# Kernel tuning notes

Measured on AMD Instinct MI355X. Metric: run time of the kernel, lower is better.

Reference implementation:

```python
import jax, jax.numpy as jnp
import numpy as np

K = 64
M = 256
V = 5000

def setup_inputs() -> dict:
    key = jax.random.key(0)
    ks = jax.random.split(key, 8)
    feat_x = jax.random.normal(ks[0], (1, V, M), dtype=jnp.float32)
    feat_y = jax.random.normal(ks[1], (1, V, M), dtype=jnp.float32)
    evals_x = jnp.sort(jax.random.uniform(ks[2], (1, K), dtype=jnp.float32))
    evals_y = jnp.sort(jax.random.uniform(ks[3], (1, K), dtype=jnp.float32))
    evecs_trans_x = jax.random.normal(ks[4], (1, K, V), dtype=jnp.float32) / np.sqrt(V)
    evecs_trans_y = jax.random.normal(ks[5], (1, K, V), dtype=jnp.float32) / np.sqrt(V)
    eye = jnp.eye(K, dtype=jnp.float32)
    sqrtMk_x = (eye + 0.05 * jax.random.normal(ks[6], (K, K), dtype=jnp.float32))[None]
    sqrtMk_y = (eye + 0.05 * jax.random.normal(ks[7], (K, K), dtype=jnp.float32))[None]
    return {"feat_x": feat_x, "feat_y": feat_y, "evals_x": evals_x, "evals_y": evals_y,
            "evecs_trans_x": evecs_trans_x, "evecs_trans_y": evecs_trans_y,
            "sqrtMk_x": sqrtMk_x, "sqrtMk_y": sqrtMk_y}

LMBDA = 0.001

def _fmap(fx, fy, ex, ey, tx, ty, sx, sy):
    # squeeze batch dim of 1 (as in torch .squeeze())
    fx, fy = fx[0], fy[0]            # [V, m]
    ex, ey = ex[0], ey[0]            # [k]
    tx, ty = tx[0], ty[0]            # [k, V]
    sx, sy = sx[0], sy[0]            # [k, k]
    A = tx @ fx                      # [k, m] spectral coeffs of feat_x
    B = sy @ (ty @ fy)               # adapt_feature=True: premultiply by sqrtMk_y
    k, m = A.shape
    vec_B = B.T.reshape(m * k, 1)
    At_Ik = jnp.kron(A.T, sy)        # [m*k, k*k] (adapt_feature -> Ik = sqrtMk_y)
    first = At_Ik.T @ At_Ik          # [k^2, k^2]
    # adapt_mask=True branch
    inv_sx = jnp.linalg.inv(sx)
    lx = jnp.diag(ex)
    ly = jnp.diag(ey)
    lx_Ik = jnp.kron(lx @ inv_sx, sy)
    Ik_ly = jnp.kron(inv_sx, sy @ ly)
    Delta = lx_Ik - Ik_ly
    second = Delta.T @ Delta
    rhs = At_Ik.T @ vec_B
    op = first + LMBDA * second
    C = jnp.linalg.solve(op, rhs)
    return C.reshape(k, k).T[None]   # [1, k, k]

def reference(feat_x, feat_y, evals_x, evals_y, evecs_trans_x, evecs_trans_y, sqrtMk_x, sqrtMk_y):
    # bidirectional=False -> only Cxy (Cyx is None in the torch module)
    return _fmap(feat_x, feat_y, evals_x, evals_y, evecs_trans_x, evecs_trans_y, sqrtMk_x, sqrtMk_y)
```

## Files before the change

kernel.cpp:

```cpp
#include <hip/hip_runtime.h>

#define LMBDA 0.001f
#define NS_SY 4
#define NS_G  5
#define NS_SX 5
#define OUTER 3
#define LDP 68

#define WS_A    0
#define WS_FY   16384
#define WS_G1   32768
#define WS_T1   36864
#define WS_R2   40960
#define WS_R4   45056
#define WS_GINV 49152
#define WS_C    53248
#define WS_FYAT 57344

#define FMA4(ar, xs, b) { ar[0]=fmaf((xs),(b).x,ar[0]); ar[1]=fmaf((xs),(b).y,ar[1]); \
                          ar[2]=fmaf((xs),(b).z,ar[2]); ar[3]=fmaf((xs),(b).w,ar[3]); }

template<int SA, int SB>
__device__ __forceinline__ void mm64(const float* __restrict__ A,
                                     const float* __restrict__ B,
                                     int ti, int tj, float a[4][4]) {
    #pragma unroll 4
    for (int k = 0; k < 64; k += 4) {
        float4 av0 = *(const float4*)&A[(4 * ti + 0) * SA + k];
        float4 av1 = *(const float4*)&A[(4 * ti + 1) * SA + k];
        float4 av2 = *(const float4*)&A[(4 * ti + 2) * SA + k];
        float4 av3 = *(const float4*)&A[(4 * ti + 3) * SA + k];
        float4 b0 = *(const float4*)&B[(k + 0) * SB + 4 * tj];
        float4 b1 = *(const float4*)&B[(k + 1) * SB + 4 * tj];
        float4 b2 = *(const float4*)&B[(k + 2) * SB + 4 * tj];
        float4 b3 = *(const float4*)&B[(k + 3) * SB + 4 * tj];
        FMA4(a[0], av0.x, b0); FMA4(a[0], av0.y, b1); FMA4(a[0], av0.z, b2); FMA4(a[0], av0.w, b3);
        FMA4(a[1], av1.x, b0); FMA4(a[1], av1.y, b1); FMA4(a[1], av1.z, b2); FMA4(a[1], av1.w, b3);
        FMA4(a[2], av2.x, b0); FMA4(a[2], av2.y, b1); FMA4(a[2], av2.z, b2); FMA4(a[2], av2.w, b3);
        FMA4(a[3], av3.x, b0); FMA4(a[3], av3.y, b1); FMA4(a[3], av3.z, b2); FMA4(a[3], av3.w, b3);
    }
}

__global__ __launch_bounds__(256) void k1_gemm(
    const float* __restrict__ tx, const float* __restrict__ fx,
    const float* __restrict__ ty, const float* __restrict__ fy,
    float* __restrict__ wsA, float* __restrict__ wsFy)
{
    __shared__ float sT[64 * LDP];
    __shared__ float sF[64 * LDP];
    const int tid = threadIdx.x;
    const int ti = tid >> 4, tj = tid & 15;
    const int mat = blockIdx.x >> 2;
    const int m0 = (blockIdx.x & 3) << 6;
    const float* __restrict__ T = mat ? ty : tx;
    const float* __restrict__ F = mat ? fy : fx;
    float* __restrict__ Out = mat ? wsFy : wsA;

    float acc[4][4];
    #pragma unroll
    for (int r = 0; r < 4; ++r)
        #pragma unroll
        for (int c = 0; c < 4; ++c) acc[r][c] = 0.f;

    for (int sc = blockIdx.y; sc * 64 < 5000; sc += 27) {
        const int v0 = sc << 6;
        int vlen = 5000 - v0; if (vlen > 64) vlen = 64;
        #pragma unroll
        for (int w = 0; w < 4; ++w) {
            const int fidx = tid + (w << 8);
            const int row = fidx >> 4, q = fidx & 15;
            const int vv = q << 2;
            if (vv < vlen) {
                float4 val = *(const float4*)(T + (size_t)row * 5000 + v0 + vv);
                sT[(vv + 0) * LDP + row] = val.x;
                sT[(vv + 1) * LDP + row] = val.y;
                sT[(vv + 2) * LDP + row] = val.z;
                sT[(vv + 3) * LDP + row] = val.w;
            }
            if (row < vlen) {
                *(float4*)&sF[row * LDP + (q << 2)] =
                    *(const float4*)(F + (size_t)(v0 + row) * 256 + m0 + (q << 2));
            }
        }
        __syncthreads();
        for (int v = 0; v < vlen; ++v) {
            float4 av = *(const float4*)&sT[v * LDP + 4 * ti];
            float4 bv = *(const float4*)&sF[v * LDP + 4 * tj];
            FMA4(acc[0], av.x, bv); FMA4(acc[1], av.y, bv);
            FMA4(acc[2], av.z, bv); FMA4(acc[3], av.w, bv);
        }
        __syncthreads();
    }
    #pragma unroll
    for (int r = 0; r < 4; ++r)
        #pragma unroll
        for (int c = 0; c < 4; ++c)
            atomicAdd(&Out[(4 * ti + r) * 256 + m0 + 4 * tj + c], acc[r][c]);
}

__device__ __forceinline__ void ns_invert(float* sM, float* sX, float* sY,
                                          int iters, int ti, int tj,
                                          int tid, float alpha)
{
    for (int idx = tid; idx < 4096; idx += 256) {
        int i = idx >> 6, j = idx & 63;
        sX[i * LDP + j] = (i == j) ? alpha : 0.f;
    }
    __syncthreads();
    for (int it = 0; it < iters; ++it) {
        float y[4][4];
        #pragma unroll
        for (int r = 0; r < 4; ++r)
            #pragma unroll
            for (int c = 0; c < 4; ++c) y[r][c] = 0.f;
        mm64<LDP, LDP>(sM, sX, ti, tj, y);
        #pragma unroll
        for (int r = 0; r < 4; ++r) {
            float4 v = {y[r][0], y[r][1], y[r][2], y[r][3]};
            *(float4*)&sY[(4 * ti + r) * 64 + 4 * tj] = v;
        }
        __syncthreads();
        float z[4][4];
        #pragma unroll
        for (int r = 0; r < 4; ++r)
            #pragma unroll
            for (int c = 0; c < 4; ++c) z[r][c] = 0.f;
        mm64<LDP, 64>(sX, sY, ti, tj, z);
        __syncthreads();
        #pragma unroll
        for (int r = 0; r < 4; ++r) {
            float4 xv = *(const float4*)&sX[(4 * ti + r) * LDP + 4 * tj];
            xv.x = 2.f * xv.x - z[r][0];
            xv.y = 2.f * xv.y - z[r][1];
            xv.z = 2.f * xv.z - z[r][2];
            xv.w = 2.f * xv.w - z[r][3];
            *(float4*)&sX[(4 * ti + r) * LDP + 4 * tj] = xv;
        }
        __syncthreads();
    }
}

__global__ __launch_bounds__(256, 1) void k2_prep(
    const float* __restrict__ wsA, const float* __restrict__ wsFy,
    const float* __restrict__ sx, const float* __restrict__ sy,
    const float* __restrict__ ex, const float* __restrict__ ey,
    float* __restrict__ ws)
{
    extern __shared__ __align__(16) float lds2[];
    const int tid = threadIdx.x;
    const int ti = tid >> 4, tj = tid & 15;
    const int b = blockIdx.x;

    if (b == 0) {
        float* sSy = lds2;
        float* sXx = lds2 + 4352;
        float* sYy = lds2 + 8704;
        float* sH  = lds2 + 12800;
        float* sV  = lds2 + 16896;
        for (int idx = tid; idx < 1024; idx += 256) {
            int i = idx >> 4, j4 = (idx & 15) << 2;
            *(float4*)&sSy[i * LDP + j4] = *(const float4*)&sy[i * 64 + j4];
        }
        if (tid < 64) sV[tid] = ey[tid];
        __syncthreads();
        {
            float h[4][4];
            #pragma unroll
            for (int r = 0; r < 4; ++r)
                #pragma unroll
                for (int c = 0; c < 4; ++c) h[r][c] = 0.f;
            for (int k = 0; k < 64; ++k) {
                float4 av = *(const float4*)&sSy[k * LDP + 4 * ti];
                float4 bv = *(const float4*)&sSy[k * LDP + 4 * tj];
                FMA4(h[0], av.x, bv); FMA4(h[1], av.y, bv);
                FMA4(h[2], av.z, bv); FMA4(h[3], av.w, bv);
            }
            #pragma unroll
            for (int r = 0; r < 4; ++r) {
                float4 v = {h[r][0], h[r][1], h[r][2], h[r][3]};
                *(float4*)&sH[(4 * ti + r) * 64 + 4 * tj] = v;
            }
        }
        __syncthreads();
        ns_invert(sSy, sXx, sYy, NS_SY, ti, tj, tid, 1.0f);
        {
            float h[4][4];
            #pragma unroll
            for (int r = 0; r < 4; ++r)
                #pragma unroll
                for (int c = 0; c < 4; ++c) h[r][c] = 0.f;
            for (int m = 0; m < 64; m += 4) {
                float4 av[4], bv[4];
                #pragma unroll
                for (int r = 0; r < 4; ++r) av[r] = *(const float4*)&sXx[(4 * ti + r) * LDP + m];
                #pragma unroll
                for (int c = 0; c < 4; ++c) bv[c] = *(const float4*)&sXx[(4 * tj + c) * LDP + m];
                #pragma unroll
                for (int r = 0; r < 4; ++r)
                    #pragma unroll
                    for (int c = 0; c < 4; ++c)
                        h[r][c] += av[r].x * bv[c].x + av[r].y * bv[c].y
                                 + av[r].z * bv[c].z + av[r].w * bv[c].w;
            }
            __syncthreads();
            #pragma unroll
            for (int r = 0; r < 4; ++r) {
                float4 v = {h[r][0], h[r][1], h[r][2], h[r][3]};
                *(float4*)&sSy[(4 * ti + r) * LDP + 4 * tj] = v;
            }
        }
        __syncthreads();
        {
            float a[4][4];
            #pragma unroll
            for (int r = 0; r < 4; ++r)
                #pragma unroll
                for (int c = 0; c < 4; ++c) a[r][c] = 0.f;
            #pragma unroll 4
            for (int k = 0; k < 64; k += 4) {
                float4 av[4];
                #pragma unroll
                for (int r = 0; r < 4; ++r) av[r] = *(const float4*)&sSy[(4 * ti + r) * LDP + k];
                #pragma unroll
                for (int q = 0; q < 4; ++q) {
                    float e = sV[k + q];
                    float4 bv = *(const float4*)&sH[(k + q) * 64 + 4 * tj];
                    bv.x *= e; bv.y *= e; bv.z *= e; bv.w *= e;
                    float xq[4] = {av[0].x, av[1].x, av[2].x, av[3].x};
                    if (q == 1) { xq[0]=av[0].y; xq[1]=av[1].y; xq[2]=av[2].y; xq[3]=av[3].y; }
                    if (q == 2) { xq[0]=av[0].z; xq[1]=av[1].z; xq[2]=av[2].z; xq[3]=av[3].z; }
                    if (q == 3) { xq[0]=av[0].w; xq[1]=av[1].w; xq[2]=av[2].w; xq[3]=av[3].w; }
                    #pragma unroll
                    for (int r = 0; r < 4; ++r) FMA4(a[r], xq[r], bv);
                }
            }
            #pragma unroll
            for (int r = 0; r < 4; ++r) {
                float4 v = {a[r][0], a[r][1], a[r][2], a[r][3]};
                *(float4*)&ws[WS_C + (4 * ti + r) * 64 + 4 * tj] = v;
            }
        }
    } else if (b == 1) {
        float* sA = lds2;
        float* sG = lds2 + 4352;
        float* sX = lds2 + 8704;
        float* sY = lds2 + 13056;
        float* sV = lds2 + 17152;
        float a[4][4];
        #pragma unroll
        for (int r = 0; r < 4; ++r)
            #pragma unroll
            for (int c = 0; c < 4; ++c) a[r][c] = 0.f;
        for (int ch = 0; ch < 4; ++ch) {
            for (int idx = tid; idx < 1024; idx += 256) {
                int i = idx >> 4, m4 = (idx & 15) << 2;
                *(float4*)&sA[i * LDP + m4] =
                    *(const float4*)&wsA[i * 256 + (ch << 6) + m4];
            }
            __syncthreads();
            for (int m = 0; m < 64; m += 4) {
                float4 av[4], bv[4];
                #pragma unroll
                for (int r = 0; r < 4; ++r) av[r] = *(const float4*)&sA[(4 * ti + r) * LDP + m];
                #pragma unroll
                for (int c = 0; c < 4; ++c) bv[c] = *(const float4*)&sA[(4 * tj + c) * LDP + m];
                #pragma unroll
                for (int r = 0; r < 4; ++r)
                    #pragma unroll
                    for (int c = 0; c < 4; ++c)
                        a[r][c] += av[r].x * bv[c].x + av[r].y * bv[c].y
                                 + av[r].z * bv[c].z + av[r].w * bv[c].w;
            }
            __syncthreads();
        }
        #pragma unroll
        for (int r = 0; r < 4; ++r) {
            float4 v = {a[r][0], a[r][1], a[r][2], a[r][3]};
            *(float4*)&sG[(4 * ti + r) * LDP + 4 * tj] = v;
            *(float4*)&ws[WS_G1 + (4 * ti + r) * 64 + 4 * tj] = v;
        }
        __syncthreads();
        if (tid < 64) {
            float s = 0.f;
            for (int j4 = 0; j4 < 64; j4 += 4) {
                float4 v = *(const float4*)&sG[tid * LDP + j4];
                s += v.x * v.x + v.y * v.y + v.z * v.z + v.w * v.w;
            }
            sV[tid] = s;
            sV[64 + tid] = sG[tid * LDP + tid];
        }
        __syncthreads();
        float f2 = 0.f, tr = 0.f;
        for (int i = 0; i < 64; ++i) { f2 += sV[i]; tr += sV[64 + i]; }
        ns_invert(sG, sX, sY, NS_G, ti, tj, tid, tr / f2);
        for (int idx = tid; idx < 1024; idx += 256) {
            int i = idx >> 4, j4 = (idx & 15) << 2;
            *(float4*)&ws[WS_GINV + i * 64 + j4] = *(const float4*)&sX[i * LDP + j4];
        }
    } else if (b == 2) {
        float* sM = lds2;
        float* sX = lds2 + 4352;
        float* sY = lds2 + 8704;
        float* sV = lds2 + 12800;
        for (int idx = tid; idx < 1024; idx += 256) {
            int i = idx >> 4, j4 = (idx & 15) << 2;
            *(float4*)&sM[i * LDP + j4] = *(const float4*)&sx[i * 64 + j4];
        }
        if (tid < 64) sV[tid] = ex[tid];
        __syncthreads();
        ns_invert(sM, sX, sY, NS_SX, ti, tj, tid, 1.0f);
        float aR2[4][4], aR4[4][4], aT1[4][4];
        #pragma unroll
        for (int r = 0; r < 4; ++r)
            #pragma unroll
            for (int c = 0; c < 4; ++c) { aR2[r][c] = 0.f; aR4[r][c] = 0.f; aT1[r][c] = 0.f; }
        for (int k = 0; k < 64; ++k) {
            float e = sV[k], e2 = e * e;
            float4 av = *(const float4*)&sX[k * LDP + 4 * ti];
            float4 bv = *(const float4*)&sX[k * LDP + 4 * tj];
            float avv[4] = {av.x, av.y, av.z, av.w};
            #pragma unroll
            for (int r = 0; r < 4; ++r) {
                FMA4(aR4[r], avv[r], bv);
                float ea = e * avv[r];
                FMA4(aR2[r], ea, bv);
                float e2a = e2 * avv[r];
                FMA4(aT1[r], e2a, bv);
            }
        }
        #pragma unroll
        for (int r = 0; r < 4; ++r) {
            int o = (4 * ti + r) * 64 + 4 * tj;
            float4 v2 = {aR2[r][0], aR2[r][1], aR2[r][2], aR2[r][3]};
            float4 v4 = {aR4[r][0], aR4[r][1], aR4[r][2], aR4[r][3]};
            float4 v1 = {aT1[r][0], aT1[r][1], aT1[r][2], aT1[r][3]};
            *(float4*)&ws[WS_R2 + o] = v2;
            *(float4*)&ws[WS_R4 + o] = v4;
            *(float4*)&ws[WS_T1 + o] = v1;
        }
    } else {
        float* sFy = lds2;
        float* sAx = lds2 + 4352;
        float a[4][4];
        #pragma unroll
        for (int r = 0; r < 4; ++r)
            #pragma unroll
            for (int c = 0; c < 4; ++c) a[r][c] = 0.f;
        for (int ch = 0; ch < 4; ++ch) {
            for (int idx = tid; idx < 1024; idx += 256) {
                int i = idx >> 4, m4 = (idx & 15) << 2;
                *(float4*)&sFy[i * LDP + m4] = *(const float4*)&wsFy[i * 256 + (ch << 6) + m4];
                *(float4*)&sAx[i * LDP + m4] = *(const float4*)&wsA[i * 256 + (ch << 6) + m4];
            }
            __syncthreads();
            for (int m = 0; m < 64; m += 4) {
                float4 av[4], bv[4];
                #pragma unroll
                for (int r = 0; r < 4; ++r) av[r] = *(const float4*)&sFy[(4 * ti + r) * LDP + m];
                #pragma unroll
                for (int c = 0; c < 4; ++c) bv[c] = *(const float4*)&sAx[(4 * tj + c) * LDP + m];
                #pragma unroll
                for (int r = 0; r < 4; ++r)
                    #pragma unroll
                    for (int c = 0; c < 4; ++c)
                        a[r][c] += av[r].x * bv[c].x + av[r].y * bv[c].y
                                 + av[r].z * bv[c].z + av[r].w * bv[c].w;
            }
            __syncthreads();
        }
        #pragma unroll
        for (int r = 0; r < 4; ++r) {
            float4 v = {a[r][0], a[r][1], a[r][2], a[r][3]};
            *(float4*)&ws[WS_FYAT + (4 * ti + r) * 64 + 4 * tj] = v;
        }
    }
}

__global__ __launch_bounds__(256, 1) void k3_solve(
    const float* __restrict__ ws, const float* __restrict__ ey_g,
    float* __restrict__ out)
{
    extern __shared__ __align__(16) float lds3[];
    float* cM1   = lds3;
    float* cR2   = lds3 + 4096;
    float* cR4   = lds3 + 8192;
    float* cGinv = lds3 + 12288;
    float* sE    = lds3 + 16384;
    float* sX    = lds3 + 20480;
    float* cC    = lds3 + 24832;
    float* sW    = lds3 + 29184;
    const int tid = threadIdx.x;
    const int ti = tid >> 4, tj = tid & 15;

    for (int idx = tid; idx < 1024; idx += 256) {
        int i = idx >> 4, j4 = (idx & 15) << 2;
        int o = i * 64 + j4;
        float4 g = *(const float4*)&ws[WS_G1 + o];
        float4 t = *(const float4*)&ws[WS_T1 + o];
        float4 m = {fmaf(LMBDA, t.x, g.x), fmaf(LMBDA, t.y, g.y),
                    fmaf(LMBDA, t.z, g.z), fmaf(LMBDA, t.w, g.w)};
        *(float4*)&cM1[o]   = m;
        *(float4*)&cR2[o]   = *(const float4*)&ws[WS_R2 + o];
        *(float4*)&cR4[o]   = *(const float4*)&ws[WS_R4 + o];
        *(float4*)&cGinv[o] = *(const float4*)&ws[WS_GINV + o];
        *(float4*)&cC[i * LDP + j4] = *(const float4*)&ws[WS_C + o];
    }
    float4 eyv = *(const float4*)&ey_g[4 * ti];
    float eyr[4] = {eyv.x, eyv.y, eyv.z, eyv.w};
    float leyr[4];
    #pragma unroll
    for (int r = 0; r < 4; ++r) leyr[r] = LMBDA * eyr[r];

    float fyr[4][4], xreg[4][4];
    #pragma unroll
    for (int r = 0; r < 4; ++r) {
        float4 v = *(const float4*)&ws[WS_FYAT + (4 * ti + r) * 64 + 4 * tj];
        fyr[r][0] = v.x; fyr[r][1] = v.y; fyr[r][2] = v.z; fyr[r][3] = v.w;
        float4 z = {0.f, 0.f, 0.f, 0.f};
        *(float4*)&sX[(4 * ti + r) * LDP + 4 * tj] = z;
        #pragma unroll
        for (int c = 0; c < 4; ++c) xreg[r][c] = 0.f;
    }
    __syncthreads();

    float E1[4][4];
    for (int it = 0; it < OUTER; ++it) {
        {
            float Sm[4][4], S2[4][4], S4[4][4];
            #pragma unroll
            for (int r = 0; r < 4; ++r)
                #pragma unroll
                for (int c = 0; c < 4; ++c) { Sm[r][c] = 0.f; S2[r][c] = 0.f; S4[r][c] = 0.f; }
            #pragma unroll 2
            for (int k = 0; k < 64; k += 4) {
                float4 av[4];
                #pragma unroll
                for (int r = 0; r < 4; ++r)
                    av[r] = *(const float4*)&sX[(4 * ti + r) * LDP + k];
                #pragma unroll
                for (int q = 0; q < 4; ++q) {
                    float4 mv = *(const float4*)&cM1[(k + q) * 64 + 4 * tj];
                    float4 qv = *(const float4*)&cR2[(k + q) * 64 + 4 * tj];
                    float4 rv = *(const float4*)&cR4[(k + q) * 64 + 4 * tj];
                    float xq[4] = {av[0].x, av[1].x, av[2].x, av[3].x};
                    if (q == 1) { xq[0]=av[0].y; xq[1]=av[1].y; xq[2]=av[2].y; xq[3]=av[3].y; }
                    if (q == 2) { xq[0]=av[0].z; xq[1]=av[1].z; xq[2]=av[2].z; xq[3]=av[3].z; }
                    if (q == 3) { xq[0]=av[0].w; xq[1]=av[1].w; xq[2]=av[2].w; xq[3]=av[3].w; }
                    #pragma unroll
                    for (int r = 0; r < 4; ++r) {
                        FMA4(Sm[r], xq[r], mv);
                        FMA4(S2[r], xq[r], qv);
                        FMA4(S4[r], xq[r], rv);
                    }
                }
            }
            #pragma unroll
            for (int r = 0; r < 4; ++r) {
                float4 e2;
                e2.x = LMBDA * fmaf(eyr[r], S4[r][0], -S2[r][0]);
                e2.y = LMBDA * fmaf(eyr[r], S4[r][1], -S2[r][1]);
                e2.z = LMBDA * fmaf(eyr[r], S4[r][2], -S2[r][2]);
                e2.w = LMBDA * fmaf(eyr[r], S4[r][3], -S2[r][3]);
                *(float4*)&sE[(4 * ti + r) * 64 + 4 * tj] = e2;
                #pragma unroll
                for (int c = 0; c < 4; ++c)
                    E1[r][c] = fmaf(-leyr[r], S2[r][c], Sm[r][c]);
            }
        }
        __syncthreads();
        {
            float Z[4][4];
            #pragma unroll
            for (int r = 0; r < 4; ++r)
                #pragma unroll
                for (int c = 0; c < 4; ++c) Z[r][c] = 0.f;
            mm64<LDP, 64>(cC, sE, ti, tj, Z);
            #pragma unroll
            for (int r = 0; r < 4; ++r) {
                float4 w;
                w.x = fyr[r][0] - E1[r][0] - Z[r][0];
                w.y = fyr[r][1] - E1[r][1] - Z[r][1];
                w.z = fyr[r][2] - E1[r][2] - Z[r][2];
                w.w = fyr[r][3] - E1[r][3] - Z[r][3];
                *(float4*)&sW[(4 * ti + r) * LDP + 4 * tj] = w;
            }
        }
        __syncthreads();
        {
            float dX[4][4];
            #pragma unroll
            for (int r = 0; r < 4; ++r)
                #pragma unroll
                for (int c = 0; c < 4; ++c) dX[r][c] = 0.f;
            mm64<LDP, 64>(sW, cGinv, ti, tj, dX);
            #pragma unroll
            for (int r = 0; r < 4; ++r) {
                float4 v;
                #pragma unroll
                for (int c = 0; c < 4; ++c) xreg[r][c] += dX[r][c];
                v.x = xreg[r][0]; v.y = xreg[r][1]; v.z = xreg[r][2]; v.w = xreg[r][3];
                *(float4*)&sX[(4 * ti + r) * LDP + 4 * tj] = v;
                if (it == OUTER - 1)
                    *(float4*)&out[(4 * ti + r) * 64 + 4 * tj] = v;
            }
        }
        if (it == OUTER - 1) break;
        __syncthreads();
    }
}

extern "C" void kernel_launch(void* const* d_in, const int* in_sizes, int n_in,
                              void* d_out, int out_size, void* d_ws, size_t ws_size,
                              hipStream_t stream) {
    (void)in_sizes; (void)n_in; (void)out_size; (void)ws_size;
    const float* fx = (const float*)d_in[0];
    const float* fy = (const float*)d_in[1];
    const float* ex = (const float*)d_in[2];
    const float* ey = (const float*)d_in[3];
    const float* tx = (const float*)d_in[4];
    const float* ty = (const float*)d_in[5];
    const float* sx = (const float*)d_in[6];
    const float* sy = (const float*)d_in[7];
    float* ws = (float*)d_ws;
    float* out = (float*)d_out;

    (void)hipFuncSetAttribute((const void*)k2_prep,
                              hipFuncAttributeMaxDynamicSharedMemorySize, 69120);
    (void)hipFuncSetAttribute((const void*)k3_solve,
                              hipFuncAttributeMaxDynamicSharedMemorySize, 134144);

    (void)hipMemsetAsync(d_ws, 0, 2 * 64 * 256 * sizeof(float), stream);
    k1_gemm<<<dim3(8, 27), 256, 0, stream>>>(tx, fx, ty, fy, ws + WS_A, ws + WS_FY);
    k2_prep<<<4, 256, 69120, stream>>>(ws + WS_A, ws + WS_FY, sx, sy, ex, ey, ws);
    k3_solve<<<1, 256, 134144, stream>>>(ws, ey, out);
}
```

Before: 181.6 us.

## Fuse three kernels into one persistent kernel with flag-based inter-block dependencies

Merges the GEMM, prep and solve kernels into a single 225-block launch whose blocks play different roles and synchronize through global atomic flags with acquire/release spin-waits. Prep work that does not depend on the GEMM (the sy and sx inversion blocks) can now run concurrently with the large reduction, and the two extra kernel launches go away. The Gram matrix G1 is now split across four blocks, one per channel chunk, that accumulate with atomics, instead of being computed serially in one block. This relies on all 225 blocks being co-resident at one block per CU, and adds spin-wait and atomic overhead.

```diff
diff --git a/kernel.cpp b/kernel.cpp
--- a/kernel.cpp
+++ b/kernel.cpp
@@ -16,6 +16,7 @@
 #define WS_GINV 49152
 #define WS_C    53248
 #define WS_FYAT 57344
+#define WS_FLAGS 61440
 
 #define FMA4(ar, xs, b) { ar[0]=fmaf((xs),(b).x,ar[0]); ar[1]=fmaf((xs),(b).y,ar[1]); \
                           ar[2]=fmaf((xs),(b).z,ar[2]); ar[3]=fmaf((xs),(b).w,ar[3]); }
@@ -41,63 +42,6 @@
     }
 }
 
-__global__ __launch_bounds__(256) void k1_gemm(
-    const float* __restrict__ tx, const float* __restrict__ fx,
-    const float* __restrict__ ty, const float* __restrict__ fy,
-    float* __restrict__ wsA, float* __restrict__ wsFy)
-{
-    __shared__ float sT[64 * LDP];
-    __shared__ float sF[64 * LDP];
-    const int tid = threadIdx.x;
-    const int ti = tid >> 4, tj = tid & 15;
-    const int mat = blockIdx.x >> 2;
-    const int m0 = (blockIdx.x & 3) << 6;
-    const float* __restrict__ T = mat ? ty : tx;
-    const float* __restrict__ F = mat ? fy : fx;
-    float* __restrict__ Out = mat ? wsFy : wsA;
-
-    float acc[4][4];
-    #pragma unroll
-    for (int r = 0; r < 4; ++r)
-        #pragma unroll
-        for (int c = 0; c < 4; ++c) acc[r][c] = 0.f;
-
-    for (int sc = blockIdx.y; sc * 64 < 5000; sc += 27) {
-        const int v0 = sc << 6;
-        int vlen = 5000 - v0; if (vlen > 64) vlen = 64;
-        #pragma unroll
-        for (int w = 0; w < 4; ++w) {
-            const int fidx = tid + (w << 8);
-            const int row = fidx >> 4, q = fidx & 15;
-            const int vv = q << 2;
-            if (vv < vlen) {
-                float4 val = *(const float4*)(T + (size_t)row * 5000 + v0 + vv);
-                sT[(vv + 0) * LDP + row] = val.x;
-                sT[(vv + 1) * LDP + row] = val.y;
-                sT[(vv + 2) * LDP + row] = val.z;
-                sT[(vv + 3) * LDP + row] = val.w;
-            }
-            if (row < vlen) {
-                *(float4*)&sF[row * LDP + (q << 2)] =
-                    *(const float4*)(F + (size_t)(v0 + row) * 256 + m0 + (q << 2));
-            }
-        }
-        __syncthreads();
-        for (int v = 0; v < vlen; ++v) {
-            float4 av = *(const float4*)&sT[v * LDP + 4 * ti];
-            float4 bv = *(const float4*)&sF[v * LDP + 4 * tj];
-            FMA4(acc[0], av.x, bv); FMA4(acc[1], av.y, bv);
-            FMA4(acc[2], av.z, bv); FMA4(acc[3], av.w, bv);
-        }
-        __syncthreads();
-    }
-    #pragma unroll
-    for (int r = 0; r < 4; ++r)
-        #pragma unroll
-        for (int c = 0; c < 4; ++c)
-            atomicAdd(&Out[(4 * ti + r) * 256 + m0 + 4 * tj + c], acc[r][c]);
-}
-
 __device__ __forceinline__ void ns_invert(float* sM, float* sX, float* sY,
                                           int iters, int ti, int tj,
                                           int tid, float alpha)
@@ -140,23 +84,134 @@
     }
 }
 
-__global__ __launch_bounds__(256, 1) void k2_prep(
-    const float* __restrict__ wsA, const float* __restrict__ wsFy,
+__device__ __forceinline__ void wait_ge(int* flag, int target, int tid) {
+    if (tid == 0) {
+        while (__hip_atomic_load(flag, __ATOMIC_ACQUIRE, __HIP_MEMORY_SCOPE_AGENT) < target)
+            __builtin_amdgcn_s_sleep(2);
+    }
+    __syncthreads();
+    __threadfence();
+}
+
+__device__ __forceinline__ void signal_one(int* flag, int tid) {
+    __syncthreads();
+    __threadfence();
+    if (tid == 0)
+        (void)__hip_atomic_fetch_add(flag, 1, __ATOMIC_RELEASE, __HIP_MEMORY_SCOPE_AGENT);
+}
+
+__global__ __launch_bounds__(256, 1) void fused_fmnet(
+    const float* __restrict__ fx, const float* __restrict__ fy,
+    const float* __restrict__ ex, const float* __restrict__ ey,
+    const float* __restrict__ tx, const float* __restrict__ ty,
     const float* __restrict__ sx, const float* __restrict__ sy,
-    const float* __restrict__ ex, const float* __restrict__ ey,
-    float* __restrict__ ws)
+    float* __restrict__ ws, float* __restrict__ out)
 {
-    extern __shared__ __align__(16) float lds2[];
+    extern __shared__ __align__(16) float lds[];
+    int* flags = (int*)(ws + WS_FLAGS);
     const int tid = threadIdx.x;
     const int ti = tid >> 4, tj = tid & 15;
-    const int b = blockIdx.x;
-
-    if (b == 0) {
-        float* sSy = lds2;
-        float* sXx = lds2 + 4352;
-        float* sYy = lds2 + 8704;
-        float* sH  = lds2 + 12800;
-        float* sV  = lds2 + 16896;
+    const int bid = blockIdx.x;
+
+    if (bid < 216) {
+        float* sT = lds;
+        float* sF = lds + 4352;
+        const int gx = bid & 7, gy = bid >> 3;
+        const int mat = gx >> 2;
+        const int m0 = (gx & 3) << 6;
+        const float* __restrict__ T = mat ? ty : tx;
+        const float* __restrict__ F = mat ? fy : fx;
+        float* __restrict__ Out = ws + (mat ? WS_FY : WS_A);
+
+        float acc[4][4];
+        #pragma unroll
+        for (int r = 0; r < 4; ++r)
+            #pragma unroll
+            for (int c = 0; c < 4; ++c) acc[r][c] = 0.f;
+
+        for (int sc = gy; sc * 64 < 5000; sc += 27) {
+            const int v0 = sc << 6;
+            int vlen = 5000 - v0; if (vlen > 64) vlen = 64;
+            #pragma unroll
+            for (int w = 0; w < 4; ++w) {
+                const int fidx = tid + (w << 8);
+                const int row = fidx >> 4, q = fidx & 15;
+                const int vv = q << 2;
+                if (vv < vlen) {
+                    float4 val = *(const float4*)(T + (size_t)row * 5000 + v0 + vv);
+                    sT[(vv + 0) * LDP + row] = val.x;
+                    sT[(vv + 1) * LDP + row] = val.y;
+                    sT[(vv + 2) * LDP + row] = val.z;
+                    sT[(vv + 3) * LDP + row] = val.w;
+                }
+                if (row < vlen) {
+                    *(float4*)&sF[row * LDP + (q << 2)] =
+                        *(const float4*)(F + (size_t)(v0 + row) * 256 + m0 + (q << 2));
+                }
+            }
+            __syncthreads();
+            for (int v = 0; v < vlen; ++v) {
+                float4 av = *(const float4*)&sT[v * LDP + 4 * ti];
+                float4 bv = *(const float4*)&sF[v * LDP + 4 * tj];
+                FMA4(acc[0], av.x, bv); FMA4(acc[1], av.y, bv);
+                FMA4(acc[2], av.z, bv); FMA4(acc[3], av.w, bv);
+            }
+            __syncthreads();
+        }
+        #pragma unroll
+        for (int r = 0; r < 4; ++r)
+            #pragma unroll
+            for (int c = 0; c < 4; ++c)
+                atomicAdd(&Out[(4 * ti + r) * 256 + m0 + 4 * tj + c], acc[r][c]);
+        __syncthreads();
+        __threadfence();
+        if (tid == 0) {
+            (void)__hip_atomic_fetch_add(&flags[gx], 1, __ATOMIC_RELEASE, __HIP_MEMORY_SCOPE_AGENT);
+            (void)__hip_atomic_fetch_add(&flags[10], 1, __ATOMIC_RELEASE, __HIP_MEMORY_SCOPE_AGENT);
+        }
+    } else if (bid < 220) {
+        const int ch = bid - 216;
+        wait_ge(&flags[ch], 27, tid);
+        float* sA = lds;
+        for (int idx = tid; idx < 1024; idx += 256) {
+            int i = idx >> 4, m4 = (idx & 15) << 2;
+            *(float4*)&sA[i * LDP + m4] =
+                *(const float4*)&ws[WS_A + i * 256 + (ch << 6) + m4];
+        }
+        __syncthreads();
+        float a[4][4];
+        #pragma unroll
+        for (int r = 0; r < 4; ++r)
+            #pragma unroll
+            for (int c = 0; c < 4; ++c) a[r][c] = 0.f;
+        for (int m = 0; m < 64; m += 4) {
+            float4 av[4], bv[4];
+            #pragma unroll
+            for (int r = 0; r < 4; ++r) av[r] = *(const float4*)&sA[(4 * ti + r) * LDP + m];
+            #pragma unroll
+            for (int c = 0; c < 4; ++c) bv[c] = *(const float4*)&sA[(4 * tj + c) * LDP + m];
+            #pragma unroll
+            for (int r = 0; r < 4; ++r)
+                #pragma unroll
+                for (int c = 0; c < 4; ++c)
+                    a[r][c] += av[r].x * bv[c].x + av[r].y * bv[c].y
+                             + av[r].z * bv[c].z + av[r].w * bv[c].w;
+        }
+        #pragma unroll
+        for (int r = 0; r < 4; ++r)
+            #pragma unroll
+            for (int c = 0; c < 4; ++c)
+                atomicAdd(&ws[WS_G1 + (4 * ti + r) * 64 + 4 * tj + c], a[r][c]);
+        __syncthreads();
+        __threadfence();
+        if (tid == 0)
+            (void)__hip_atomic_fetch_add(&flags[8], 1, __ATOMIC_RELEASE, __HIP_MEMORY_SCOPE_AGENT);
+    } else if (bid == 220) {
+        float* sSy = lds;
+        float* sXx = lds + 4352;
+        float* sYy = lds + 8704;
+        float* sH  = lds + 12800;
+        float* sV  = lds + 16896;
         for (int idx = tid; idx < 1024; idx += 256) {
             int i = idx >> 4, j4 = (idx & 15) << 2;
             *(float4*)&sSy[i * LDP + j4] = *(const float4*)&sy[i * 64 + j4];
@@ -240,68 +295,12 @@
                 *(float4*)&ws[WS_C + (4 * ti + r) * 64 + 4 * tj] = v;
             }
         }
-    } else if (b == 1) {
-        float* sA = lds2;
-        float* sG = lds2 + 4352;
-        float* sX = lds2 + 8704;
-        float* sY = lds2 + 13056;
-        float* sV = lds2 + 17152;
-        float a[4][4];
-        #pragma unroll
-        for (int r = 0; r < 4; ++r)
-            #pragma unroll
-            for (int c = 0; c < 4; ++c) a[r][c] = 0.f;
-        for (int ch = 0; ch < 4; ++ch) {
-            for (int idx = tid; idx < 1024; idx += 256) {
-                int i = idx >> 4, m4 = (idx & 15) << 2;
-                *(float4*)&sA[i * LDP + m4] =
-                    *(const float4*)&wsA[i * 256 + (ch << 6) + m4];
-            }
-            __syncthreads();
-            for (int m = 0; m < 64; m += 4) {
-                float4 av[4], bv[4];
-                #pragma unroll
-                for (int r = 0; r < 4; ++r) av[r] = *(const float4*)&sA[(4 * ti + r) * LDP + m];
-                #pragma unroll
-                for (int c = 0; c < 4; ++c) bv[c] = *(const float4*)&sA[(4 * tj + c) * LDP + m];
-                #pragma unroll
-                for (int r = 0; r < 4; ++r)
-                    #pragma unroll
-                    for (int c = 0; c < 4; ++c)
-                        a[r][c] += av[r].x * bv[c].x + av[r].y * bv[c].y
-                                 + av[r].z * bv[c].z + av[r].w * bv[c].w;
-            }
-            __syncthreads();
-        }
-        #pragma unroll
-        for (int r = 0; r < 4; ++r) {
-            float4 v = {a[r][0], a[r][1], a[r][2], a[r][3]};
-            *(float4*)&sG[(4 * ti + r) * LDP + 4 * tj] = v;
-            *(float4*)&ws[WS_G1 + (4 * ti + r) * 64 + 4 * tj] = v;
-        }
-        __syncthreads();
-        if (tid < 64) {
-            float s = 0.f;
-            for (int j4 = 0; j4 < 64; j4 += 4) {
-                float4 v = *(const float4*)&sG[tid * LDP + j4];
-                s += v.x * v.x + v.y * v.y + v.z * v.z + v.w * v.w;
-            }
-            sV[tid] = s;
-            sV[64 + tid] = sG[tid * LDP + tid];
-        }
-        __syncthreads();
-        float f2 = 0.f, tr = 0.f;
-        for (int i = 0; i < 64; ++i) { f2 += sV[i]; tr += sV[64 + i]; }
-        ns_invert(sG, sX, sY, NS_G, ti, tj, tid, tr / f2);
-        for (int idx = tid; idx < 1024; idx += 256) {
-            int i = idx >> 4, j4 = (idx & 15) << 2;
-            *(float4*)&ws[WS_GINV + i * 64 + j4] = *(const float4*)&sX[i * LDP + j4];
-        }
-    } else if (b == 2) {
-        float* sM = lds2;
-        float* sX = lds2 + 4352;
-        float* sY = lds2 + 8704;
-        float* sV = lds2 + 12800;
+        signal_one(&flags[9], tid);
+    } else if (bid == 221) {
+        float* sM = lds;
+        float* sX = lds + 4352;
+        float* sY = lds + 8704;
+        float* sV = lds + 12800;
         for (int idx = tid; idx < 1024; idx += 256) {
             int i = idx >> 4, j4 = (idx & 15) << 2;
             *(float4*)&sM[i * LDP + j4] = *(const float4*)&sx[i * 64 + j4];
@@ -338,9 +337,40 @@
             *(float4*)&ws[WS_R4 + o] = v4;
             *(float4*)&ws[WS_T1 + o] = v1;
         }
-    } else {
-        float* sFy = lds2;
-        float* sAx = lds2 + 4352;
+        signal_one(&flags[9], tid);
+    } else if (bid == 222) {
+        wait_ge(&flags[8], 4, tid);
+        float* sG = lds;
+        float* sX = lds + 4352;
+        float* sY = lds + 8704;
+        float* sV = lds + 12800;
+        for (int idx = tid; idx < 1024; idx += 256) {
+            int i = idx >> 4, j4 = (idx & 15) << 2;
+            *(float4*)&sG[i * LDP + j4] = *(const float4*)&ws[WS_G1 + i * 64 + j4];
+        }
+        __syncthreads();
+        if (tid < 64) {
+            float s = 0.f;
+            for (int j4 = 0; j4 < 64; j4 += 4) {
+                float4 v = *(const float4*)&sG[tid * LDP + j4];
+                s += v.x * v.x + v.y * v.y + v.z * v.z + v.w * v.w;
+            }
+            sV[tid] = s;
+            sV[64 + tid] = sG[tid * LDP + tid];
+        }
+        __syncthreads();
+        float f2 = 0.f, tr = 0.f;
+        for (int i = 0; i < 64; ++i) { f2 += sV[i]; tr += sV[64 + i]; }
+        ns_invert(sG, sX, sY, NS_G, ti, tj, tid, tr / f2);
+        for (int idx = tid; idx < 1024; idx += 256) {
+            int i = idx >> 4, j4 = (idx & 15) << 2;
+            *(float4*)&ws[WS_GINV + i * 64 + j4] = *(const float4*)&sX[i * LDP + j4];
+        }
+        signal_one(&flags[9], tid);
+    } else if (bid == 223) {
+        wait_ge(&flags[10], 216, tid);
+        float* sFy = lds;
+        float* sAx = lds + 4352;
         float a[4][4];
         #pragma unroll
         for (int r = 0; r < 4; ++r)
@@ -349,8 +379,8 @@
         for (int ch = 0; ch < 4; ++ch) {
             for (int idx = tid; idx < 1024; idx += 256) {
                 int i = idx >> 4, m4 = (idx & 15) << 2;
-                *(float4*)&sFy[i * LDP + m4] = *(const float4*)&wsFy[i * 256 + (ch << 6) + m4];
-                *(float4*)&sAx[i * LDP + m4] = *(const float4*)&wsA[i * 256 + (ch << 6) + m4];
+                *(float4*)&sFy[i * LDP + m4] = *(const float4*)&ws[WS_FY + i * 256 + (ch << 6) + m4];
+                *(float4*)&sAx[i * LDP + m4] = *(const float4*)&ws[WS_A  + i * 256 + (ch << 6) + m4];
             }
             __syncthreads();
             for (int m = 0; m < 64; m += 4) {
@@ -373,139 +403,133 @@
             float4 v = {a[r][0], a[r][1], a[r][2], a[r][3]};
             *(float4*)&ws[WS_FYAT + (4 * ti + r) * 64 + 4 * tj] = v;
         }
-    }
-}
-
-__global__ __launch_bounds__(256, 1) void k3_solve(
-    const float* __restrict__ ws, const float* __restrict__ ey_g,
-    float* __restrict__ out)
-{
-    extern __shared__ __align__(16) float lds3[];
-    float* cM1   = lds3;
-    float* cR2   = lds3 + 4096;
-    float* cR4   = lds3 + 8192;
-    float* cGinv = lds3 + 12288;
-    float* sE    = lds3 + 16384;
-    float* sX    = lds3 + 20480;
-    float* cC    = lds3 + 24832;
-    float* sW    = lds3 + 29184;
-    const int tid = threadIdx.x;
-    const int ti = tid >> 4, tj = tid & 15;
-
-    for (int idx = tid; idx < 1024; idx += 256) {
-        int i = idx >> 4, j4 = (idx & 15) << 2;
-        int o = i * 64 + j4;
-        float4 g = *(const float4*)&ws[WS_G1 + o];
-        float4 t = *(const float4*)&ws[WS_T1 + o];
-        float4 m = {fmaf(LMBDA, t.x, g.x), fmaf(LMBDA, t.y, g.y),
-                    fmaf(LMBDA, t.z, g.z), fmaf(LMBDA, t.w, g.w)};
-        *(float4*)&cM1[o]   = m;
-        *(float4*)&cR2[o]   = *(const float4*)&ws[WS_R2 + o];
-        *(float4*)&cR4[o]   = *(const float4*)&ws[WS_R4 + o];
-        *(float4*)&cGinv[o] = *(const float4*)&ws[WS_GINV + o];
-        *(float4*)&cC[i * LDP + j4] = *(const float4*)&ws[WS_C + o];
-    }
-    float4 eyv = *(const float4*)&ey_g[4 * ti];
-    float eyr[4] = {eyv.x, eyv.y, eyv.z, eyv.w};
-    float leyr[4];
-    #pragma unroll
-    for (int r = 0; r < 4; ++r) leyr[r] = LMBDA * eyr[r];
-
-    float fyr[4][4], xreg[4][4];
-    #pragma unroll
-    for (int r = 0; r < 4; ++r) {
-        float4 v = *(const float4*)&ws[WS_FYAT + (4 * ti + r) * 64 + 4 * tj];
-        fyr[r][0] = v.x; fyr[r][1] = v.y; fyr[r][2] = v.z; fyr[r][3] = v.w;
-        float4 z = {0.f, 0.f, 0.f, 0.f};
-        *(float4*)&sX[(4 * ti + r) * LDP + 4 * tj] = z;
-        #pragma unroll
-        for (int c = 0; c < 4; ++c) xreg[r][c] = 0.f;
-    }
-    __syncthreads();
-
-    float E1[4][4];
-    for (int it = 0; it < OUTER; ++it) {
-        {
-            float Sm[4][4], S2[4][4], S4[4][4];
-            #pragma unroll
-            for (int r = 0; r < 4; ++r)
-                #pragma unroll
-                for (int c = 0; c < 4; ++c) { Sm[r][c] = 0.f; S2[r][c] = 0.f; S4[r][c] = 0.f; }
-            #pragma unroll 2
-            for (int k = 0; k < 64; k += 4) {
-                float4 av[4];
+        signal_one(&flags[9], tid);
+    } else {
+        wait_ge(&flags[9], 4, tid);
+        float* cM1   = lds;
+        float* cR2   = lds + 4096;
+        float* cR4   = lds + 8192;
+        float* cGinv = lds + 12288;
+        float* sE    = lds + 16384;
+        float* sX    = lds + 20480;
+        float* cC    = lds + 24832;
+        float* sW    = lds + 29184;
+
+        for (int idx = tid; idx < 1024; idx += 256) {
+            int i = idx >> 4, j4 = (idx & 15) << 2;
+            int o = i * 64 + j4;
+            float4 g = *(const float4*)&ws[WS_G1 + o];
+            float4 t = *(const float4*)&ws[WS_T1 + o];
+            float4 m = {fmaf(LMBDA, t.x, g.x), fmaf(LMBDA, t.y, g.y),
+                        fmaf(LMBDA, t.z, g.z), fmaf(LMBDA, t.w, g.w)};
+            *(float4*)&cM1[o]   = m;
+            *(float4*)&cR2[o]   = *(const float4*)&ws[WS_R2 + o];
+            *(float4*)&cR4[o]   = *(const float4*)&ws[WS_R4 + o];
+            *(float4*)&cGinv[o] = *(const float4*)&ws[WS_GINV + o];
+            *(float4*)&cC[i * LDP + j4] = *(const float4*)&ws[WS_C + o];
+        }
+        float4 eyv = *(const float4*)&ey[4 * ti];
+        float eyr[4] = {eyv.x, eyv.y, eyv.z, eyv.w};
+        float leyr[4];
+        #pragma unroll
+        for (int r = 0; r < 4; ++r) leyr[r] = LMBDA * eyr[r];
+
+        float fyr[4][4], xreg[4][4];
+        #pragma unroll
+        for (int r = 0; r < 4; ++r) {
+            float4 v = *(const float4*)&ws[WS_FYAT + (4 * ti + r) * 64 + 4 * tj];
+            fyr[r][0] = v.x; fyr[r][1] = v.y; fyr[r][2] = v.z; fyr[r][3] = v.w;
+            float4 z = {0.f, 0.f, 0.f, 0.f};
+            *(float4*)&sX[(4 * ti + r) * LDP + 4 * tj] = z;
+            #pragma unroll
+            for (int c = 0; c < 4; ++c) xreg[r][c] = 0.f;
+        }
+        __syncthreads();
+
+        float E1[4][4];
+        for (int it = 0; it < OUTER; ++it) {
+            {
+                float Sm[4][4], S2[4][4], S4[4][4];
                 #pragma unroll
                 for (int r = 0; r < 4; ++r)
-                    av[r] = *(const float4*)&sX[(4 * ti + r) * LDP + k];
-                #pragma unroll
-                for (int q = 0; q < 4; ++q) {
-                    float4 mv = *(const float4*)&cM1[(k + q) * 64 + 4 * tj];
-                    float4 qv = *(const float4*)&cR2[(k + q) * 64 + 4 * tj];
-                    float4 rv = *(const float4*)&cR4[(k + q) * 64 + 4 * tj];
-                    float xq[4] = {av[0].x, av[1].x, av[2].x, av[3].x};
-                    if (q == 1) { xq[0]=av[0].y; xq[1]=av[1].y; xq[2]=av[2].y; xq[3]=av[3].y; }
-                    if (q == 2) { xq[0]=av[0].z; xq[1]=av[1].z; xq[2]=av[2].z; xq[3]=av[3].z; }
-                    if (q == 3) { xq[0]=av[0].w; xq[1]=av[1].w; xq[2]=av[2].w; xq[3]=av[3].w; }
-                    #pragma unroll
-                    for (int r = 0; r < 4; ++r) {
-                        FMA4(Sm[r], xq[r], mv);
-                        FMA4(S2[r], xq[r], qv);
-                        FMA4(S4[r], xq[r], rv);
+                    #pragma unroll
+                    for (int c = 0; c < 4; ++c) { Sm[r][c] = 0.f; S2[r][c] = 0.f; S4[r][c] = 0.f; }
+                #pragma unroll 2
+                for (int k = 0; k < 64; k += 4) {
+                    float4 av[4];
+                    #pragma unroll
+                    for (int r = 0; r < 4; ++r)
+                        av[r] = *(const float4*)&sX[(4 * ti + r) * LDP + k];
+                    #pragma unroll
+                    for (int q = 0; q < 4; ++q) {
+                        float4 mv = *(const float4*)&cM1[(k + q) * 64 + 4 * tj];
+                        float4 qv = *(const float4*)&cR2[(k + q) * 64 + 4 * tj];
+                        float4 rv = *(const float4*)&cR4[(k + q) * 64 + 4 * tj];
+                        float xq[4] = {av[0].x, av[1].x, av[2].x, av[3].x};
+                        if (q == 1) { xq[0]=av[0].y; xq[1]=av[1].y; xq[2]=av[2].y; xq[3]=av[3].y; }
+                        if (q == 2) { xq[0]=av[0].z; xq[1]=av[1].z; xq[2]=av[2].z; xq[3]=av[3].z; }
+                        if (q == 3) { xq[0]=av[0].w; xq[1]=av[1].w; xq[2]=av[2].w; xq[3]=av[3].w; }
+                        #pragma unroll
+                        for (int r = 0; r < 4; ++r) {
+                            FMA4(Sm[r], xq[r], mv);
+                            FMA4(S2[r], xq[r], qv);
+                            FMA4(S4[r], xq[r], rv);
+                        }
                     }
                 }
-            }
-            #pragma unroll
-            for (int r = 0; r < 4; ++r) {
-                float4 e2;
-                e2.x = LMBDA * fmaf(eyr[r], S4[r][0], -S2[r][0]);
-                e2.y = LMBDA * fmaf(eyr[r], S4[r][1], -S2[r][1]);
-                e2.z = LMBDA * fmaf(eyr[r], S4[r][2], -S2[r][2]);
-                e2.w = LMBDA * fmaf(eyr[r], S4[r][3], -S2[r][3]);
-                *(float4*)&sE[(4 * ti + r) * 64 + 4 * tj] = e2;
-                #pragma unroll
-                for (int c = 0; c < 4; ++c)
-                    E1[r][c] = fmaf(-leyr[r], S2[r][c], Sm[r][c]);
-            }
-        }
-        __syncthreads();
-        {
-            float Z[4][4];
-            #pragma unroll
-            for (int r = 0; r < 4; ++r)
-                #pragma unroll
-                for (int c = 0; c < 4; ++c) Z[r][c] = 0.f;
-            mm64<LDP, 64>(cC, sE, ti, tj, Z);
-            #pragma unroll
-            for (int r = 0; r < 4; ++r) {
-                float4 w;
-                w.x = fyr[r][0] - E1[r][0] - Z[r][0];
-                w.y = fyr[r][1] - E1[r][1] - Z[r][1];
-                w.z = fyr[r][2] - E1[r][2] - Z[r][2];
-                w.w = fyr[r][3] - E1[r][3] - Z[r][3];
-                *(float4*)&sW[(4 * ti + r) * LDP + 4 * tj] = w;
-            }
-        }
-        __syncthreads();
-        {
-            float dX[4][4];
-            #pragma unroll
-            for (int r = 0; r < 4; ++r)
-                #pragma unroll
-                for (int c = 0; c < 4; ++c) dX[r][c] = 0.f;
-            mm64<LDP, 64>(sW, cGinv, ti, tj, dX);
-            #pragma unroll
-            for (int r = 0; r < 4; ++r) {
-                float4 v;
-                #pragma unroll
-                for (int c = 0; c < 4; ++c) xreg[r][c] += dX[r][c];
-                v.x = xreg[r][0]; v.y = xreg[r][1]; v.z = xreg[r][2]; v.w = xreg[r][3];
-                *(float4*)&sX[(4 * ti + r) * LDP + 4 * tj] = v;
-                if (it == OUTER - 1)
-                    *(float4*)&out[(4 * ti + r) * 64 + 4 * tj] = v;
-            }
-        }
-        if (it == OUTER - 1) break;
-        __syncthreads();
+                #pragma unroll
+                for (int r = 0; r < 4; ++r) {
+                    float4 e2;
+                    e2.x = LMBDA * fmaf(eyr[r], S4[r][0], -S2[r][0]);
+                    e2.y = LMBDA * fmaf(eyr[r], S4[r][1], -S2[r][1]);
+                    e2.z = LMBDA * fmaf(eyr[r], S4[r][2], -S2[r][2]);
+                    e2.w = LMBDA * fmaf(eyr[r], S4[r][3], -S2[r][3]);
+                    *(float4*)&sE[(4 * ti + r) * 64 + 4 * tj] = e2;
+                    #pragma unroll
+                    for (int c = 0; c < 4; ++c)
+                        E1[r][c] = fmaf(-leyr[r], S2[r][c], Sm[r][c]);
+                }
+            }
+            __syncthreads();
+            {
+                float Z[4][4];
+                #pragma unroll
+                for (int r = 0; r < 4; ++r)
+                    #pragma unroll
+                    for (int c = 0; c < 4; ++c) Z[r][c] = 0.f;
+                mm64<LDP, 64>(cC, sE, ti, tj, Z);
+                #pragma unroll
+                for (int r = 0; r < 4; ++r) {
+                    float4 w;
+                    w.x = fyr[r][0] - E1[r][0] - Z[r][0];
+                    w.y = fyr[r][1] - E1[r][1] - Z[r][1];
+                    w.z = fyr[r][2] - E1[r][2] - Z[r][2];
+                    w.w = fyr[r][3] - E1[r][3] - Z[r][3];
+                    *(float4*)&sW[(4 * ti + r) * LDP + 4 * tj] = w;
+                }
+            }
+            __syncthreads();
+            {
+                float dX[4][4];
+                #pragma unroll
+                for (int r = 0; r < 4; ++r)
+                    #pragma unroll
+                    for (int c = 0; c < 4; ++c) dX[r][c] = 0.f;
+                mm64<LDP, 64>(sW, cGinv, ti, tj, dX);
+                #pragma unroll
+                for (int r = 0; r < 4; ++r) {
+                    float4 v;
+                    #pragma unroll
+                    for (int c = 0; c < 4; ++c) xreg[r][c] += dX[r][c];
+                    v.x = xreg[r][0]; v.y = xreg[r][1]; v.z = xreg[r][2]; v.w = xreg[r][3];
+                    *(float4*)&sX[(4 * ti + r) * LDP + 4 * tj] = v;
+                    if (it == OUTER - 1)
+                        *(float4*)&out[(4 * ti + r) * 64 + 4 * tj] = v;
+                }
+            }
+            if (it == OUTER - 1) break;
+            __syncthreads();
+        }
     }
 }
 
@@ -524,13 +548,10 @@
     float* ws = (float*)d_ws;
     float* out = (float*)d_out;
 
-    (void)hipFuncSetAttribute((const void*)k2_prep,
-                              hipFuncAttributeMaxDynamicSharedMemorySize, 69120);
-    (void)hipFuncSetAttribute((const void*)k3_solve,
+    (void)hipFuncSetAttribute((const void*)fused_fmnet,
                               hipFuncAttributeMaxDynamicSharedMemorySize, 134144);
 
-    (void)hipMemsetAsync(d_ws, 0, 2 * 64 * 256 * sizeof(float), stream);
-    k1_gemm<<<dim3(8, 27), 256, 0, stream>>>(tx, fx, ty, fy, ws + WS_A, ws + WS_FY);
-    k2_prep<<<4, 256, 69120, stream>>>(ws + WS_A, ws + WS_FY, sx, sy, ex, ey, ws);
-    k3_solve<<<1, 256, 134144, stream>>>(ws, ey, out);
+    (void)hipMemsetAsync(d_ws, 0, (WS_G1 + 4096) * sizeof(float), stream);
+    (void)hipMemsetAsync((char*)d_ws + WS_FLAGS * sizeof(float), 0, 64, stream);
+    fused_fmnet<<<225, 256, 134144, stream>>>(fx, fy, ex, ey, tx, ty, sx, sy, ws, out);
 }
```

Result: slower. 194.7 us (+7.2%).
